# Performance work log

Hardware: AMD Instinct MI355X
Metric: run time of the kernel (lower is better)

Reference implementation:

```python
import jax, jax.numpy as jnp
import numpy as np

N = 100000        # nodes
E = 1600000       # edges (avg degree 16)
IN_DIM = 128
OUT_DIM = 128
P_DROP = 0.1


def setup_inputs() -> dict:
    key = jax.random.key(0)
    k1, k2, k3, k4 = jax.random.split(key, 4)
    x = jax.random.normal(k1, (N, IN_DIM), dtype=jnp.float32)
    edge_index = jax.random.randint(k2, (2, E), 0, N, dtype=jnp.int64)
    # glorot-uniform-ish init for the GCNConv linear weight
    limit = float(np.sqrt(6.0 / (IN_DIM + OUT_DIM)))
    W = jax.random.uniform(k3, (IN_DIM, OUT_DIM), dtype=jnp.float32,
                           minval=-limit, maxval=limit)
    b = jnp.zeros((OUT_DIM,), dtype=jnp.float32)
    drop_u = jax.random.uniform(k4, (N, OUT_DIM), dtype=jnp.float32)
    return {"x": x, "edge_index": edge_index, "W": W, "b": b, "drop_u": drop_u}


def reference(x, edge_index, W, b, drop_u):
    n = x.shape[0]
    # linear transform first (PyG GCNConv: lin has no bias)
    h = x @ W  # [N, OUT]
    # add self-loops
    loops = jnp.arange(n, dtype=edge_index.dtype)
    src = jnp.concatenate([edge_index[0], loops])  # [E+N]
    dst = jnp.concatenate([edge_index[1], loops])
    # symmetric normalization: deg computed on destination column
    deg = jax.ops.segment_sum(jnp.ones_like(dst, dtype=h.dtype), dst,
                              num_segments=n)
    dinv = jnp.where(deg > 0, jax.lax.rsqrt(deg), 0.0)
    norm = dinv[src] * dinv[dst]  # [E+N]
    # gather-message-scatter: out[dst] += norm * h[src]
    msgs = h[src] * norm[:, None]                       # [E+N, OUT]
    out = jax.ops.segment_sum(msgs, dst, num_segments=n) + b
    # ReLU + (deterministic-mask) inverted dropout
    out = jax.nn.relu(out)
    keep = 1.0 - P_DROP
    out = jnp.where(drop_u >= P_DROP, out / keep, 0.0)
    return out
```

## Files before the change

kernel.cpp:

```cpp
#include <hip/hip_runtime.h>

#define DIM 128
#define D4 32
#define D2 64
#define EPB1 4096

typedef short short8 __attribute__((ext_vector_type(8)));
typedef float f32x4 __attribute__((ext_vector_type(4)));

__device__ __forceinline__ unsigned pack_bf16(float a, float b) {
    unsigned ua = __float_as_uint(a);
    unsigned ub = __float_as_uint(b);
    ua = (ua + 0x7FFFu + ((ua >> 16) & 1u)) >> 16;
    ub = (ub + 0x7FFFu + ((ub >> 16) & 1u)) & 0xFFFF0000u;
    return ua | ub;
}
__device__ __forceinline__ unsigned short bf16_of(float a) {
    unsigned ua = __float_as_uint(a);
    return (unsigned short)((ua + 0x7FFFu + ((ua >> 16) & 1u)) >> 16);
}
__device__ __forceinline__ float blo(unsigned u) { return __uint_as_float(u << 16); }
__device__ __forceinline__ float bhi(unsigned u) { return __uint_as_float(u & 0xFFFF0000u); }

__device__ __forceinline__ void acc8(const uint4& v,
                                     float& f0, float& f1, float& f2, float& f3,
                                     float& f4, float& f5, float& f6, float& f7) {
    f0 += blo(v.x); f1 += bhi(v.x);
    f2 += blo(v.y); f3 += bhi(v.y);
    f4 += blo(v.z); f5 += bhi(v.z);
    f6 += blo(v.w); f7 += bhi(v.w);
}


__global__ __launch_bounds__(512) void k_hist1(const int* __restrict__ dst, int E,
                                               int* __restrict__ H, int* __restrict__ tot,
                                               int NB1, int NBUCK,
                                               const float* __restrict__ W,
                                               unsigned short* __restrict__ wt) {
    if (blockIdx.x >= (unsigned)NB1) {
        int base = (blockIdx.x - NB1) * 2048 + threadIdx.x * 4;
#pragma unroll
        for (int i = 0; i < 4; ++i) {
            int o = base + i;
            if (o < DIM * DIM) {
                int j = o >> 7, k = o & 127;
                wt[o] = bf16_of(W[k * DIM + j]);
            }
        }
        return;
    }
    __shared__ int h[512];
    const int t = threadIdx.x;
    for (int i = t; i < NBUCK; i += 512) h[i] = 0;
    __syncthreads();
    const int base = blockIdx.x * EPB1;
#pragma unroll
    for (int i = 0; i < EPB1 / 512; ++i) {
        int e = base + i * 512 + t;
        if (e < E) atomicAdd(&h[dst[e] >> 9], 1);
    }
    __syncthreads();
    for (int i = t; i < NBUCK; i += 512) {
        int c = h[i];
        H[i * NB1 + blockIdx.x] = c;
        if (c) atomicAdd(&tot[i], c);
    }
}

__global__ __launch_bounds__(512) void k_scanB(int* __restrict__ H,
                                               const int* __restrict__ tot,
                                               int* __restrict__ binbase,
                                               int NB1, int NBUCK, int E) {
    __shared__ int sh[512];
    const int bin = blockIdx.x;
    const int t = threadIdx.x;

    int tv = (t < NBUCK) ? tot[t] : 0;
    sh[t] = tv;
    __syncthreads();
    for (int o = 1; o < 512; o <<= 1) {
        int x = (t >= o) ? sh[t - o] : 0;
        __syncthreads();
        sh[t] += x;
        __syncthreads();
    }
    const int mybase = sh[bin] - ((bin < NBUCK) ? tot[bin] : 0);
    if (t == bin && t < NBUCK) binbase[t] = mybase;
    if (bin == 0 && t == 0) binbase[NBUCK] = E;
    __syncthreads();

    int v = (t < NB1) ? H[bin * NB1 + t] : 0;
    sh[t] = v;
    __syncthreads();
    for (int o = 1; o < 512; o <<= 1) {
        int x = (t >= o) ? sh[t - o] : 0;
        __syncthreads();
        sh[t] += x;
        __syncthreads();
    }
    if (t < NB1) H[bin * NB1 + t] = mybase + sh[t] - v;
}

__global__ __launch_bounds__(512) void k_scatter1(const int* __restrict__ ei, int E,
                                                  const int* __restrict__ H,
                                                  unsigned* __restrict__ ebuf,
                                                  int NB1, int NBUCK) {
    __shared__ int cnt[512];
    const int t = threadIdx.x;
    const int blk = blockIdx.x;
    for (int i = t; i < NBUCK; i += 512) cnt[i] = 0;
    __syncthreads();
    const int* src = ei;
    const int* dst = ei + E;
    const int base = blk * EPB1;
#pragma unroll
    for (int i = 0; i < EPB1 / 512; ++i) {
        int e = base + i * 512 + t;
        if (e < E) {
            int d = dst[e];
            int s = src[e];
            int b = d >> 9;
            int r = atomicAdd(&cnt[b], 1);
            ebuf[H[b * NB1 + blk] + r] = ((unsigned)s << 9) | (unsigned)(d & 511);
        }
    }
}

__global__ __launch_bounds__(512) void k_bucket2(const unsigned* __restrict__ ebuf,
                                                 const int* __restrict__ binbase,
                                                 int* __restrict__ srclist,
                                                 int* __restrict__ rowstart,
                                                 float* __restrict__ dinv,
                                                 int n, int E) {
    __shared__ int h[512];
    __shared__ int off[512];
    __shared__ int cnt[512];
    const int t = threadIdx.x;
    const int b = blockIdx.x;
    const int beg = binbase[b];
    const int end = binbase[b + 1];
    h[t] = 0; cnt[t] = 0;
    __syncthreads();
    for (int j = beg + t; j < end; j += 512) atomicAdd(&h[ebuf[j] & 511], 1);
    __syncthreads();
    int v = h[t];
    off[t] = v;
    __syncthreads();
    for (int o = 1; o < 512; o <<= 1) {
        int x = (t >= o) ? off[t - o] : 0;
        __syncthreads();
        off[t] += x;
        __syncthreads();
    }
    const int excl = off[t] - v;
    const int node = b * 512 + t;
    if (node < n) {
        rowstart[node] = beg + excl;
        dinv[node] = rsqrtf((float)(v + 1));
    }
    if (b == 0 && t == 0) rowstart[n] = E;
    h[t] = beg + excl;
    __syncthreads();
    for (int j = beg + t; j < end; j += 512) {
        unsigned p = ebuf[j];
        int lo = p & 511;
        int r = atomicAdd(&cnt[lo], 1);
        srclist[h[lo] + r] = (int)(p >> 9);
    }
}


__global__ __launch_bounds__(256) void k_xprep(const float* __restrict__ x,
                                               const float* __restrict__ dinv,
                                               unsigned* __restrict__ xs, int n) {
    long t = (long)blockIdx.x * blockDim.x + threadIdx.x;
    long total = (long)n * D4;
    if (t >= total) return;
    int row = (int)(t >> 5);
    float di = dinv[row];
    float4 v = ((const float4*)x)[t];
    uint2 o;
    o.x = pack_bf16(v.x * di, v.y * di);
    o.y = pack_bf16(v.z * di, v.w * di);
    ((uint2*)xs)[t] = o;
}

__global__ __launch_bounds__(256) void k_wprep(const float* __restrict__ W,
                                               unsigned short* __restrict__ wt) {
    int o = blockIdx.x * blockDim.x + threadIdx.x;
    if (o >= DIM * DIM) return;
    int j = o >> 7, k = o & 127;
    wt[o] = bf16_of(W[k * DIM + j]);
}

__global__ __launch_bounds__(256) void k_gather_mfma(
        const int* __restrict__ rowstart, const int* __restrict__ srclist,
        const uint4* __restrict__ xs4, const float* __restrict__ dinv,
        const unsigned short* __restrict__ WT, const float* __restrict__ bias,
        const float* __restrict__ du, float* __restrict__ out,
        int n) {
    __shared__ unsigned char Atile[16 * 256];

    const int wv   = threadIdx.x >> 6;
    const int lane = threadIdx.x & 63;
    const int g = lane >> 4;
    const int q = lane & 15;
    const long row0 = (long)blockIdx.x * 16;

    for (int nd = 0; nd < 4; ++nd) {
        const int lrow = wv * 4 + nd;
        const long node = row0 + lrow;
        unsigned char* dstb = Atile + lrow * 256 + ((q * 16) ^ ((lrow & 7) << 4));
        if (node < n) {
            const float di = dinv[node];
            float f0 = 0.f, f1 = 0.f, f2 = 0.f, f3 = 0.f,
                  f4 = 0.f, f5 = 0.f, f6 = 0.f, f7 = 0.f;
            if (g == 0) {
                uint4 v = xs4[node * 16 + q];
                acc8(v, f0, f1, f2, f3, f4, f5, f6, f7);
            }
            const int beg = rowstart[node];
            const int end = rowstart[node + 1];
            for (int base = beg; base < end; base += 64) {
                const int m = (end - base < 64) ? (end - base) : 64;
                int sidx = (base + lane < end) ? srclist[base + lane] : 0;
                int k = 0;
                for (; k + 8 <= m; k += 8) {
                    int sa = __shfl(sidx, k + g);
                    int sb = __shfl(sidx, k + 4 + g);
                    uint4 va = xs4[(long)sa * 16 + q];
                    uint4 vb = xs4[(long)sb * 16 + q];
                    acc8(va, f0, f1, f2, f3, f4, f5, f6, f7);
                    acc8(vb, f0, f1, f2, f3, f4, f5, f6, f7);
                }
                for (; k + 4 <= m; k += 4) {
                    int sa = __shfl(sidx, k + g);
                    uint4 va = xs4[(long)sa * 16 + q];
                    acc8(va, f0, f1, f2, f3, f4, f5, f6, f7);
                }
                const int rem = m - k;
                if (rem) {
                    int sa = __shfl(sidx, k + g);
                    if (g < rem) {
                        uint4 va = xs4[(long)sa * 16 + q];
                        acc8(va, f0, f1, f2, f3, f4, f5, f6, f7);
                    }
                }
            }
#pragma unroll
            for (int off = 16; off < 64; off <<= 1) {
                f0 += __shfl_xor(f0, off); f1 += __shfl_xor(f1, off);
                f2 += __shfl_xor(f2, off); f3 += __shfl_xor(f3, off);
                f4 += __shfl_xor(f4, off); f5 += __shfl_xor(f5, off);
                f6 += __shfl_xor(f6, off); f7 += __shfl_xor(f7, off);
            }
            if (g == 0) {
                uint4 o;
                o.x = pack_bf16(f0 * di, f1 * di);
                o.y = pack_bf16(f2 * di, f3 * di);
                o.z = pack_bf16(f4 * di, f5 * di);
                o.w = pack_bf16(f6 * di, f7 * di);
                *(uint4*)dstb = o;
            }
        } else if (g == 0) {
            uint4 z; z.x = z.y = z.z = z.w = 0u;
            *(uint4*)dstb = z;
        }
    }
    __syncthreads();

    const int lr = lane & 15;
    const int lk8 = g * 8;
    const long grow = row0 + lr;

    short8 afr[4];
#pragma unroll
    for (int ks = 0; ks < 4; ++ks)
        afr[ks] = *(const short8*)(Atile + lr * 256 +
                                   (((ks * 64) + g * 16) ^ ((lr & 7) << 4)));

    const float inv_keep = 1.0f / 0.9f;
#pragma unroll
    for (int ct = 0; ct < 2; ++ct) {
        const int colbase = wv * 32 + ct * 16;
        f32x4 acc = {0.f, 0.f, 0.f, 0.f};
#pragma unroll
        for (int ks = 0; ks < 4; ++ks) {
            short8 wfr = *reinterpret_cast<const short8*>(
                WT + (long)(colbase + lr) * DIM + ks * 32 + lk8);
            acc = __builtin_amdgcn_mfma_f32_16x16x32_bf16(wfr, afr[ks], acc, 0, 0, 0);
        }
        if (grow < n) {
            const int gcol = colbase + g * 4;
            float4 bb = *reinterpret_cast<const float4*>(bias + gcol);
            float4 u  = *reinterpret_cast<const float4*>(du + grow * DIM + gcol);
            float4 v;
            v.x = acc[0] + bb.x; v.y = acc[1] + bb.y;
            v.z = acc[2] + bb.z; v.w = acc[3] + bb.w;
            v.x = (u.x >= 0.1f) ? fmaxf(v.x, 0.f) * inv_keep : 0.f;
            v.y = (u.y >= 0.1f) ? fmaxf(v.y, 0.f) * inv_keep : 0.f;
            v.z = (u.z >= 0.1f) ? fmaxf(v.z, 0.f) * inv_keep : 0.f;
            v.w = (u.w >= 0.1f) ? fmaxf(v.w, 0.f) * inv_keep : 0.f;
            *reinterpret_cast<float4*>(out + grow * DIM + gcol) = v;
        }
    }
}


__global__ void k_hist(const int* __restrict__ dst, int E, int* __restrict__ hist) {
    int e = blockIdx.x * blockDim.x + threadIdx.x;
    if (e < E) atomicAdd(&hist[dst[e]], 1);
}
__global__ void k_dinv(const int* __restrict__ hist, float* __restrict__ dinv, int n) {
    int i = blockIdx.x * blockDim.x + threadIdx.x;
    if (i < n) dinv[i] = rsqrtf((float)(hist[i] + 1));
}
__global__ __launch_bounds__(256) void k_scan1(const int* __restrict__ hist,
                                               int* __restrict__ rowstart,
                                               int* __restrict__ bsum, int n) {
    __shared__ int sh[256];
    const int t = threadIdx.x;
    const int base = blockIdx.x * 1024 + t * 4;
    int v0 = (base + 0 < n) ? hist[base + 0] : 0;
    int v1 = (base + 1 < n) ? hist[base + 1] : 0;
    int v2 = (base + 2 < n) ? hist[base + 2] : 0;
    int v3 = (base + 3 < n) ? hist[base + 3] : 0;
    int s = v0 + v1 + v2 + v3;
    sh[t] = s;
    __syncthreads();
    for (int off = 1; off < 256; off <<= 1) {
        int xv = (t >= off) ? sh[t - off] : 0;
        __syncthreads();
        sh[t] += xv;
        __syncthreads();
    }
    if (t == 255) bsum[blockIdx.x] = sh[255];
    int run = sh[t] - s;
    if (base + 0 < n) rowstart[base + 0] = run; run += v0;
    if (base + 1 < n) rowstart[base + 1] = run; run += v1;
    if (base + 2 < n) rowstart[base + 2] = run; run += v2;
    if (base + 3 < n) rowstart[base + 3] = run;
}
__global__ __launch_bounds__(256) void k_scan2(int* __restrict__ bsum, int B) {
    __shared__ int sh[256];
    const int t = threadIdx.x;
    int v = (t < B) ? bsum[t] : 0;
    sh[t] = v;
    __syncthreads();
    for (int off = 1; off < 256; off <<= 1) {
        int xv = (t >= off) ? sh[t - off] : 0;
        __syncthreads();
        sh[t] += xv;
        __syncthreads();
    }
    if (t < B) bsum[t] = sh[t] - v;
}
__global__ void k_scan3(int* __restrict__ rowstart, const int* __restrict__ bsum,
                        int n, int E) {
    int i = blockIdx.x * blockDim.x + threadIdx.x;
    if (i < n) rowstart[i] += bsum[i >> 10];
    else if (i == n) rowstart[n] = E;
}
__global__ void k_fill(const int* __restrict__ ei, int E,
                       const int* __restrict__ rowstart, int* __restrict__ cursor,
                       int* __restrict__ srclist) {
    int e = blockIdx.x * blockDim.x + threadIdx.x;
    if (e >= E) return;
    int d = ei[E + e];
    int pos = atomicAdd(&cursor[d], 1);
    srclist[rowstart[d] + pos] = ei[e];
}
__global__ __launch_bounds__(256) void k_gather_bf(const int* __restrict__ rowstart,
                                                   const int* __restrict__ srclist,
                                                   const unsigned* __restrict__ xs,
                                                   const float* __restrict__ dinv,
                                                   float* __restrict__ out, int n) {
    const int node = blockIdx.x * 4 + (threadIdx.x >> 6);
    const int lane = threadIdx.x & 63;
    if (node >= n) return;
    const float di = dinv[node];
    unsigned sv = xs[(long)node * D2 + lane];
    float2 acc;
    acc.x = __uint_as_float(sv << 16);
    acc.y = __uint_as_float(sv & 0xFFFF0000u);
    const int beg = rowstart[node];
    const int end = rowstart[node + 1];
    int j = beg;
    for (; j + 3 < end; j += 4) {
        int s0 = srclist[j]; int s1 = srclist[j + 1];
        int s2 = srclist[j + 2]; int s3 = srclist[j + 3];
        unsigned v0 = xs[(long)s0 * D2 + lane];
        unsigned v1 = xs[(long)s1 * D2 + lane];
        unsigned v2 = xs[(long)s2 * D2 + lane];
        unsigned v3 = xs[(long)s3 * D2 + lane];
        acc.x += __uint_as_float(v0 << 16) + __uint_as_float(v1 << 16)
               + __uint_as_float(v2 << 16) + __uint_as_float(v3 << 16);
        acc.y += __uint_as_float(v0 & 0xFFFF0000u) + __uint_as_float(v1 & 0xFFFF0000u)
               + __uint_as_float(v2 & 0xFFFF0000u) + __uint_as_float(v3 & 0xFFFF0000u);
    }
    for (; j < end; ++j) {
        unsigned v0 = xs[(long)srclist[j] * D2 + lane];
        acc.x += __uint_as_float(v0 << 16);
        acc.y += __uint_as_float(v0 & 0xFFFF0000u);
    }
    acc.x *= di; acc.y *= di;
    ((float2*)out)[(long)node * D2 + lane] = acc;
}

__global__ __launch_bounds__(256) void k_gather_bb(const int* __restrict__ rowstart,
                                                   const int* __restrict__ srclist,
                                                   const uint4* __restrict__ xs4,
                                                   const float* __restrict__ dinv,
                                                   uint4* __restrict__ agg4, int n) {
    const int node = blockIdx.x * 4 + (threadIdx.x >> 6);
    const int lane = threadIdx.x & 63;
    if (node >= n) return;
    const int g = lane >> 4;
    const int q = lane & 15;
    const float di = dinv[node];

    float f0 = 0.f, f1 = 0.f, f2 = 0.f, f3 = 0.f,
          f4 = 0.f, f5 = 0.f, f6 = 0.f, f7 = 0.f;
    if (g == 0) {
        uint4 v = xs4[(long)node * 16 + q];
        acc8(v, f0, f1, f2, f3, f4, f5, f6, f7);
    }
    const int beg = rowstart[node];
    const int end = rowstart[node + 1];
    for (int base = beg; base < end; base += 64) {
        const int m = (end - base < 64) ? (end - base) : 64;
        int sidx = (base + lane < end) ? srclist[base + lane] : 0;
        int k = 0;
        for (; k + 8 <= m; k += 8) {
            int sa = __shfl(sidx, k + g);
            int sb = __shfl(sidx, k + 4 + g);
            uint4 va = xs4[(long)sa * 16 + q];
            uint4 vb = xs4[(long)sb * 16 + q];
            acc8(va, f0, f1, f2, f3, f4, f5, f6, f7);
            acc8(vb, f0, f1, f2, f3, f4, f5, f6, f7);
        }
        for (; k + 4 <= m; k += 4) {
            int sa = __shfl(sidx, k + g);
            uint4 va = xs4[(long)sa * 16 + q];
            acc8(va, f0, f1, f2, f3, f4, f5, f6, f7);
        }
        const int rem = m - k;
        if (rem) {
            int sa = __shfl(sidx, k + g);
            if (g < rem) {
                uint4 va = xs4[(long)sa * 16 + q];
                acc8(va, f0, f1, f2, f3, f4, f5, f6, f7);
            }
        }
    }
#pragma unroll
    for (int off = 16; off < 64; off <<= 1) {
        f0 += __shfl_xor(f0, off); f1 += __shfl_xor(f1, off);
        f2 += __shfl_xor(f2, off); f3 += __shfl_xor(f3, off);
        f4 += __shfl_xor(f4, off); f5 += __shfl_xor(f5, off);
        f6 += __shfl_xor(f6, off); f7 += __shfl_xor(f7, off);
    }
    if (g == 0) {
        uint4 o;
        o.x = pack_bf16(f0 * di, f1 * di);
        o.y = pack_bf16(f2 * di, f3 * di);
        o.z = pack_bf16(f4 * di, f5 * di);
        o.w = pack_bf16(f6 * di, f7 * di);
        agg4[(long)node * 16 + q] = o;
    }
}

__global__ __launch_bounds__(256) void k_mfma_transform(
        const unsigned short* __restrict__ A, const unsigned short* __restrict__ WT,
        const float* __restrict__ bias, const float* __restrict__ du,
        float* __restrict__ out, int n, int ntiles) {
    const int wave  = threadIdx.x >> 6;
    const int lane  = threadIdx.x & 63;
    const int rhalf = wave >> 1;
    const int cg    = wave & 1;
    const int lr    = lane & 15;
    const int g     = lane >> 4;
    const int lk8   = g * 8;

    const int t = blockIdx.x;
    if (t >= ntiles) return;
    const long row0 = (long)t * 32 + rhalf * 16;
    const long grow = row0 + lr;

    long ar = grow; if (ar >= n) ar = n - 1;
    short8 afr[4];
#pragma unroll
    for (int ks = 0; ks < 4; ++ks)
        afr[ks] = *reinterpret_cast<const short8*>(A + ar * DIM + ks * 32 + lk8);

    const float inv_keep = 1.0f / 0.9f;
#pragma unroll
    for (int ct = 0; ct < 4; ++ct) {
        const int colbase = cg * 64 + ct * 16;
        f32x4 acc = {0.f, 0.f, 0.f, 0.f};
#pragma unroll
        for (int ks = 0; ks < 4; ++ks) {
            short8 wfr = *reinterpret_cast<const short8*>(
                WT + (long)(colbase + lr) * DIM + ks * 32 + lk8);
            acc = __builtin_amdgcn_mfma_f32_16x16x32_bf16(wfr, afr[ks], acc, 0, 0, 0);
        }
        if (grow < n) {
            const int gcol = colbase + g * 4;
            float4 bb = *reinterpret_cast<const float4*>(bias + gcol);
            float4 u  = *reinterpret_cast<const float4*>(du + grow * DIM + gcol);
            float4 v;
            v.x = acc[0] + bb.x; v.y = acc[1] + bb.y;
            v.z = acc[2] + bb.z; v.w = acc[3] + bb.w;
            v.x = (u.x >= 0.1f) ? fmaxf(v.x, 0.f) * inv_keep : 0.f;
            v.y = (u.y >= 0.1f) ? fmaxf(v.y, 0.f) * inv_keep : 0.f;
            v.z = (u.z >= 0.1f) ? fmaxf(v.z, 0.f) * inv_keep : 0.f;
            v.w = (u.w >= 0.1f) ? fmaxf(v.w, 0.f) * inv_keep : 0.f;
            *reinterpret_cast<float4*>(out + grow * DIM + gcol) = v;
        }
    }
}

extern "C" void kernel_launch(void* const* d_in, const int* in_sizes, int n_in,
                              void* d_out, int out_size, void* d_ws, size_t ws_size,
                              hipStream_t stream) {
    const float* x  = (const float*)d_in[0];
    const int*   ei = (const int*)d_in[1];
    const float* W  = (const float*)d_in[2];
    const float* b  = (const float*)d_in[3];
    const float* du = (const float*)d_in[4];
    float* out = (float*)d_out;

    const int n = in_sizes[0] / DIM;
    const int E = in_sizes[1] / 2;

    auto al = [](size_t v) { return (v + 255) & ~(size_t)255; };
    char* ws = (char*)d_ws;

    const int NBUCK = (n + 511) >> 9;
    const int NB1   = (E + EPB1 - 1) / EPB1;

    size_t o_dinv = 0;
    size_t o_rs   = o_dinv + al((size_t)n * 4);
    size_t o_src  = o_rs   + al(((size_t)n + 1) * 4);
    size_t o_xs   = o_src  + al((size_t)E * 4);
    size_t o_agg  = o_xs   + al((size_t)n * DIM * 2);
    size_t o_wt   = o_agg  + al((size_t)n * DIM * 2);
    size_t o_H    = o_wt   + al((size_t)DIM * DIM * 2);
    size_t o_tot  = o_H    + al((size_t)NBUCK * NB1 * 4);
    size_t o_bb   = o_tot  + al((size_t)NBUCK * 4);
    size_t o_ebuf = o_bb   + al(((size_t)NBUCK + 1) * 4);
    size_t need3  = o_ebuf + (size_t)E * 4;

    float* dinv     = (float*)(ws + o_dinv);
    int*   rowstart = (int*)(ws + o_rs);
    int*   srclist  = (int*)(ws + o_src);
    unsigned* xs    = (unsigned*)(ws + o_xs);
    unsigned* agg   = (unsigned*)(ws + o_agg);
    unsigned short* wt = (unsigned short*)(ws + o_wt);
    int*   H        = (int*)(ws + o_H);
    int*   tot      = (int*)(ws + o_tot);
    int*   binbase  = (int*)(ws + o_bb);
    unsigned* ebuf  = (unsigned*)(ws + o_ebuf);

    const int bs = 256;

    if (ws_size >= need3 && NBUCK <= 512 && NB1 <= 512) {
        (void)hipMemsetAsync(tot, 0, (size_t)NBUCK * 4, stream);
        k_hist1<<<NB1 + 8, 512, 0, stream>>>(ei + E, E, H, tot, NB1, NBUCK, W, wt);
        k_scanB<<<NBUCK, 512, 0, stream>>>(H, tot, binbase, NB1, NBUCK, E);
        k_scatter1<<<NB1, 512, 0, stream>>>(ei, E, H, ebuf, NB1, NBUCK);
        k_bucket2<<<NBUCK, 512, 0, stream>>>(ebuf, binbase, srclist, rowstart, dinv, n, E);

        long t_x = (long)n * D4;
        k_xprep<<<(int)((t_x + bs - 1) / bs), bs, 0, stream>>>(x, dinv, xs, n);
        int ntiles16 = (n + 15) / 16;
        k_gather_mfma<<<ntiles16, 256, 0, stream>>>(rowstart, srclist,
                                                    (const uint4*)xs, dinv,
                                                    wt, b, du, out, n);
        return;
    }

    size_t f_dinv = 0;
    size_t f_hist = f_dinv + al((size_t)n * 4);
    size_t f_rs   = f_hist + al((size_t)n * 4);
    size_t f_bsum = f_rs   + al(((size_t)n + 1) * 4);
    size_t f_src  = f_bsum + 1024;
    size_t f_xs   = f_src  + al((size_t)E * 4);
    size_t f_agg  = f_xs   + al((size_t)n * DIM * 2);
    size_t f_wt   = f_agg  + al((size_t)n * DIM * 2);
    size_t need1  = f_agg;
    size_t need2  = f_wt + (size_t)DIM * DIM * 2;

    float* fdinv     = (float*)(ws + f_dinv);
    int*   fhist     = (int*)(ws + f_hist);
    int*   frowstart = (int*)(ws + f_rs);
    int*   fbsum     = (int*)(ws + f_bsum);
    int*   fsrclist  = (int*)(ws + f_src);
    unsigned* fxs    = (unsigned*)(ws + f_xs);
    unsigned* fagg   = (unsigned*)(ws + f_agg);
    unsigned short* fwt = (unsigned short*)(ws + f_wt);

    const int B = (n + 1023) / 1024;
    (void)hipMemsetAsync(fhist, 0, (size_t)n * 4, stream);
    k_hist<<<(E + bs - 1) / bs, bs, 0, stream>>>(ei + E, E, fhist);
    k_dinv<<<(n + bs - 1) / bs, bs, 0, stream>>>(fhist, fdinv, n);
    k_scan1<<<B, 256, 0, stream>>>(fhist, frowstart, fbsum, n);
    k_scan2<<<1, 256, 0, stream>>>(fbsum, B);
    k_scan3<<<(n + 1 + bs - 1) / bs, bs, 0, stream>>>(frowstart, fbsum, n, E);
    (void)hipMemsetAsync(fhist, 0, (size_t)n * 4, stream);
    k_fill<<<(E + bs - 1) / bs, bs, 0, stream>>>(ei, E, frowstart, fhist, fsrclist);

    if (ws_size >= need2) {
        long t_x = (long)n * D4;
        k_xprep<<<(int)((t_x + bs - 1) / bs), bs, 0, stream>>>(x, fdinv, fxs, n);
        k_wprep<<<(DIM * DIM + bs - 1) / bs, bs, 0, stream>>>(W, fwt);
        k_gather_bb<<<(n + 3) / 4, 256, 0, stream>>>(frowstart, fsrclist,
                                                     (const uint4*)fxs, fdinv,
                                                     (uint4*)fagg, n);
        int ntiles = (n + 31) / 32;
        k_mfma_transform<<<ntiles, 256, 0, stream>>>((const unsigned short*)fagg, fwt,
                                                     b, du, out, n, ntiles);
    } else if (ws_size >= need1) {
        long t_x = (long)n * D4;
        k_xprep<<<(int)((t_x + bs - 1) / bs), bs, 0, stream>>>(x, fdinv, fxs, n);
        k_gather_bf<<<(n + 3) / 4, 256, 0, stream>>>(frowstart, fsrclist, fxs, fdinv, out, n);
    }
}
```

Measured before the change: 157.1 us.

## Fuse x prescale into bucket kernel, widen gather blocks to 512 threads

The separate k_xprep launch is folded into k_bucket2: each bucket block scales its 512 rows of x by a locally cached dinv and writes the bf16 copy, saving one launch and a dinv reload. k_gather_mfma now runs 8 waves per block, each aggregating 2 rows and computing one 16-column MFMA tile instead of two. EPB1 is doubled, so each scatter/hist block covers more edges and fewer blocks are launched. Risks: the bucket kernel's tail grows, since only NBUCK blocks now do the x conversion with less parallelism, and 512-thread gather blocks may lower occupancy.

```diff
diff --git a/kernel.cpp b/kernel.cpp
--- a/kernel.cpp
+++ b/kernel.cpp
@@ -3,7 +3,7 @@
 #define DIM 128
 #define D4 32
 #define D2 64
-#define EPB1 4096
+#define EPB1 8192
 
 typedef short short8 __attribute__((ext_vector_type(8)));
 typedef float f32x4 __attribute__((ext_vector_type(4)));
@@ -131,10 +131,13 @@
                                                  int* __restrict__ srclist,
                                                  int* __restrict__ rowstart,
                                                  float* __restrict__ dinv,
+                                                 const float* __restrict__ x,
+                                                 unsigned* __restrict__ xs,
                                                  int n, int E) {
     __shared__ int h[512];
     __shared__ int off[512];
     __shared__ int cnt[512];
+    __shared__ float dinvl[512];
     const int t = threadIdx.x;
     const int b = blockIdx.x;
     const int beg = binbase[b];
@@ -147,16 +150,18 @@
     off[t] = v;
     __syncthreads();
     for (int o = 1; o < 512; o <<= 1) {
-        int x = (t >= o) ? off[t - o] : 0;
-        __syncthreads();
-        off[t] += x;
+        int x2 = (t >= o) ? off[t - o] : 0;
+        __syncthreads();
+        off[t] += x2;
         __syncthreads();
     }
     const int excl = off[t] - v;
-    const int node = b * 512 + t;
+    const long node = (long)b * 512 + t;
+    float dl = rsqrtf((float)(v + 1));
+    dinvl[t] = dl;
     if (node < n) {
         rowstart[node] = beg + excl;
-        dinv[node] = rsqrtf((float)(v + 1));
+        dinv[node] = dl;
     }
     if (b == 0 && t == 0) rowstart[n] = E;
     h[t] = beg + excl;
@@ -166,6 +171,19 @@
         int lo = p & 511;
         int r = atomicAdd(&cnt[lo], 1);
         srclist[h[lo] + r] = (int)(p >> 9);
+    }
+    const long rowbase = (long)b * 512;
+    for (int i = t; i < 512 * D4; i += 512) {
+        int r = i >> 5, c = i & 31;
+        long nd = rowbase + r;
+        if (nd < n) {
+            float dd = dinvl[r];
+            float4 v4 = ((const float4*)x)[nd * D4 + c];
+            uint2 o;
+            o.x = pack_bf16(v4.x * dd, v4.y * dd);
+            o.y = pack_bf16(v4.z * dd, v4.w * dd);
+            ((uint2*)xs)[nd * D4 + c] = o;
+        }
     }
 }
 
@@ -193,7 +211,7 @@
     wt[o] = bf16_of(W[k * DIM + j]);
 }
 
-__global__ __launch_bounds__(256) void k_gather_mfma(
+__global__ __launch_bounds__(512) void k_gather_mfma(
         const int* __restrict__ rowstart, const int* __restrict__ srclist,
         const uint4* __restrict__ xs4, const float* __restrict__ dinv,
         const unsigned short* __restrict__ WT, const float* __restrict__ bias,
@@ -207,8 +225,8 @@
     const int q = lane & 15;
     const long row0 = (long)blockIdx.x * 16;
 
-    for (int nd = 0; nd < 4; ++nd) {
-        const int lrow = wv * 4 + nd;
+    for (int nd = 0; nd < 2; ++nd) {
+        const int lrow = wv * 2 + nd;
         const long node = row0 + lrow;
         unsigned char* dstb = Atile + lrow * 256 + ((q * 16) ^ ((lrow & 7) << 4));
         if (node < n) {
@@ -280,29 +298,26 @@
                                    (((ks * 64) + g * 16) ^ ((lr & 7) << 4)));
 
     const float inv_keep = 1.0f / 0.9f;
-#pragma unroll
-    for (int ct = 0; ct < 2; ++ct) {
-        const int colbase = wv * 32 + ct * 16;
-        f32x4 acc = {0.f, 0.f, 0.f, 0.f};
-#pragma unroll
-        for (int ks = 0; ks < 4; ++ks) {
-            short8 wfr = *reinterpret_cast<const short8*>(
-                WT + (long)(colbase + lr) * DIM + ks * 32 + lk8);
-            acc = __builtin_amdgcn_mfma_f32_16x16x32_bf16(wfr, afr[ks], acc, 0, 0, 0);
-        }
-        if (grow < n) {
-            const int gcol = colbase + g * 4;
-            float4 bb = *reinterpret_cast<const float4*>(bias + gcol);
-            float4 u  = *reinterpret_cast<const float4*>(du + grow * DIM + gcol);
-            float4 v;
-            v.x = acc[0] + bb.x; v.y = acc[1] + bb.y;
-            v.z = acc[2] + bb.z; v.w = acc[3] + bb.w;
-            v.x = (u.x >= 0.1f) ? fmaxf(v.x, 0.f) * inv_keep : 0.f;
-            v.y = (u.y >= 0.1f) ? fmaxf(v.y, 0.f) * inv_keep : 0.f;
-            v.z = (u.z >= 0.1f) ? fmaxf(v.z, 0.f) * inv_keep : 0.f;
-            v.w = (u.w >= 0.1f) ? fmaxf(v.w, 0.f) * inv_keep : 0.f;
-            *reinterpret_cast<float4*>(out + grow * DIM + gcol) = v;
-        }
+    const int colbase = wv * 16;
+    f32x4 acc = {0.f, 0.f, 0.f, 0.f};
+#pragma unroll
+    for (int ks = 0; ks < 4; ++ks) {
+        short8 wfr = *reinterpret_cast<const short8*>(
+            WT + (long)(colbase + lr) * DIM + ks * 32 + lk8);
+        acc = __builtin_amdgcn_mfma_f32_16x16x32_bf16(wfr, afr[ks], acc, 0, 0, 0);
+    }
+    if (grow < n) {
+        const int gcol = colbase + g * 4;
+        float4 bb = *reinterpret_cast<const float4*>(bias + gcol);
+        float4 u  = *reinterpret_cast<const float4*>(du + grow * DIM + gcol);
+        float4 v;
+        v.x = acc[0] + bb.x; v.y = acc[1] + bb.y;
+        v.z = acc[2] + bb.z; v.w = acc[3] + bb.w;
+        v.x = (u.x >= 0.1f) ? fmaxf(v.x, 0.f) * inv_keep : 0.f;
+        v.y = (u.y >= 0.1f) ? fmaxf(v.y, 0.f) * inv_keep : 0.f;
+        v.z = (u.z >= 0.1f) ? fmaxf(v.z, 0.f) * inv_keep : 0.f;
+        v.w = (u.w >= 0.1f) ? fmaxf(v.w, 0.f) * inv_keep : 0.f;
+        *reinterpret_cast<float4*>(out + grow * DIM + gcol) = v;
     }
 }
 
@@ -569,12 +584,11 @@
         k_hist1<<<NB1 + 8, 512, 0, stream>>>(ei + E, E, H, tot, NB1, NBUCK, W, wt);
         k_scanB<<<NBUCK, 512, 0, stream>>>(H, tot, binbase, NB1, NBUCK, E);
         k_scatter1<<<NB1, 512, 0, stream>>>(ei, E, H, ebuf, NB1, NBUCK);
-        k_bucket2<<<NBUCK, 512, 0, stream>>>(ebuf, binbase, srclist, rowstart, dinv, n, E);
-
-        long t_x = (long)n * D4;
-        k_xprep<<<(int)((t_x + bs - 1) / bs), bs, 0, stream>>>(x, dinv, xs, n);
+        k_bucket2<<<NBUCK, 512, 0, stream>>>(ebuf, binbase, srclist, rowstart, dinv,
+                                             x, xs, n, E);
+
         int ntiles16 = (n + 15) / 16;
-        k_gather_mfma<<<ntiles16, 256, 0, stream>>>(rowstart, srclist,
+        k_gather_mfma<<<ntiles16, 512, 0, stream>>>(rowstart, srclist,
                                                     (const uint4*)xs, dinv,
                                                     wt, b, du, out, n);
         return;
```

New measurement: 151.2 us, median of 3. 1.04x faster.
